# Kernel optimization log

Hardware: AMD Instinct MI355X
Metric: run time of the kernel (lower is better)

## Reference

```python
import jax, jax.numpy as jnp
import numpy as np

H = 8
DH = 64
MAX_REL = 32
SCALE = DH ** -0.5


def setup_inputs() -> dict:
    key = jax.random.key(0)
    ks = jax.random.split(key, 10)
    B, T, D = 2, 2048, 512
    s = 1.0 / np.sqrt(D)
    return {
        "hidden_states": jax.random.normal(ks[0], (B, T, D), jnp.float32),
        "Wq": jax.random.normal(ks[1], (D, H * DH), jnp.float32) * s,
        "bq": jax.random.normal(ks[2], (H * DH,), jnp.float32) * 0.02,
        "Wk": jax.random.normal(ks[3], (D, H * DH), jnp.float32) * s,
        "bk": jax.random.normal(ks[4], (H * DH,), jnp.float32) * 0.02,
        "Wv": jax.random.normal(ks[5], (D, H * DH), jnp.float32) * s,
        "bv": jax.random.normal(ks[6], (H * DH,), jnp.float32) * 0.02,
        "Wo": jax.random.normal(ks[7], (H * DH, D), jnp.float32) * s,
        "bo": jax.random.normal(ks[8], (D,), jnp.float32) * 0.02,
        "rel_bias": jax.random.normal(ks[9], (H, 2 * MAX_REL + 1), jnp.float32) * 0.02,
    }


def _rel_pos_bias(rel_bias, Tq, Tk):
    # (H, Tq, Tk) additive bias from clamped relative distances
    rel = jnp.arange(Tq)[:, None] - jnp.arange(Tk)[None, :]
    idx = jnp.clip(rel, -MAX_REL, MAX_REL) + MAX_REL
    return rel_bias[:, idx]


def reference(hidden_states, Wq, bq, Wk, bk, Wv, bv, Wo, bo, rel_bias):
    B, T, D = hidden_states.shape
    # projections (enn.Linear == dense linear map in forward math)
    Q = (hidden_states @ Wq + bq).reshape(B, T, H, DH)
    K = (hidden_states @ Wk + bk).reshape(B, T, H, DH)
    V = (hidden_states @ Wv + bv).reshape(B, T, H, DH)
    attn = jnp.einsum("bthd,bkhd->bhtk", Q, K) * SCALE
    attn = attn + _rel_pos_bias(rel_bias, T, T)[None]
    attn = jax.nn.softmax(attn, axis=-1)
    out = jnp.einsum("bhtk,bkhd->bthd", attn, V).reshape(B, T, H * DH)
    return out @ Wo + bo
```

## Files before the change

kernel.cpp:

```cpp
#include <hip/hip_runtime.h>
#include <stdint.h>
#include <math.h>

#define H 8
#define DH 64
#define T 2048
#define D 512
#define B 2
#define BH 16
#define MAXREL 32
#define NREL (2*MAXREL+1)
#define C1 0.18033688f
#define NKIT 16

typedef _Float16 half_t;
typedef half_t half8 __attribute__((ext_vector_type(8)));
typedef float f32x4 __attribute__((ext_vector_type(4)));

typedef __attribute__((address_space(3))) unsigned int lds_uint;
typedef const __attribute__((address_space(1))) unsigned int glb_uint;

__device__ __forceinline__ void gl_lds16(const void* g, void* l) {
    __builtin_amdgcn_global_load_lds((glb_uint*)g, (lds_uint*)l, 16, 0, 0);
}

__device__ __forceinline__ f32x4 zero4() { f32x4 z = {0.f, 0.f, 0.f, 0.f}; return z; }

__global__ __launch_bounds__(256) void cvt_x(const float* __restrict__ X,
                                             half_t* __restrict__ Xh) {
    const int i = (blockIdx.x * 256 + threadIdx.x) * 8;
    const float4 a = *(const float4*)(X + i);
    const float4 b = *(const float4*)(X + i + 4);
    half8 o;
    o[0]=(half_t)a.x; o[1]=(half_t)a.y; o[2]=(half_t)a.z; o[3]=(half_t)a.w;
    o[4]=(half_t)b.x; o[5]=(half_t)b.y; o[6]=(half_t)b.z; o[7]=(half_t)b.w;
    *(half8*)(Xh + i) = o;
}

__global__ __launch_bounds__(256) void trans_w(
    const float* __restrict__ Wq, const float* __restrict__ Wk,
    const float* __restrict__ Wv, const float* __restrict__ Wo,
    half_t* __restrict__ Wts) {
    const int z = blockIdx.y;
    const float* __restrict__ W = (z==0)?Wq:(z==1)?Wk:(z==2)?Wv:Wo;
    half_t* __restrict__ out = Wts + (size_t)z * (D * D);

    __shared__ half_t Ld[64 * 72];
    const int tid = threadIdx.x;
    const int k0 = (blockIdx.x >> 3) * 64;
    const int n0 = (blockIdx.x & 7) * 64;
    const int r = tid >> 2, c16 = (tid & 3) * 16;

    const float* src = W + (size_t)(k0 + r) * D + n0 + c16;
    #pragma unroll
    for (int j = 0; j < 16; ++j) Ld[r * 72 + c16 + j] = (half_t)src[j];
    __syncthreads();
    half_t tmp[16];
    #pragma unroll
    for (int j = 0; j < 16; ++j) tmp[j] = Ld[(c16 + j) * 72 + r];
    half8* dst = (half8*)(out + (size_t)(n0 + r) * D + k0 + c16);
    dst[0] = *(half8*)&tmp[0];
    dst[1] = *(half8*)&tmp[8];
}

__global__ __launch_bounds__(256) void gemm_qkv(
    const half_t* __restrict__ Xh, const half_t* __restrict__ Wts,
    const float* __restrict__ bq, const float* __restrict__ bk,
    const float* __restrict__ bv,
    half_t* __restrict__ Qh, half_t* __restrict__ Kh, half_t* __restrict__ Vh)
{
    __shared__ half_t As[64 * 32];
    __shared__ half_t Bs[128 * 32];
    const int tid = threadIdx.x, w = tid >> 6, lane = tid & 63;
    const int l15 = lane & 15, quad = lane >> 4;
    const int m0 = blockIdx.x * 64, n0 = blockIdx.y * 128, z = blockIdx.z;
    const half_t* __restrict__ Wt = Wts + (size_t)z * (D * D);
    const float* __restrict__ bias = (z==0)?bq:(z==1)?bk:bv;
    half_t* __restrict__ dst = (z==0)?Qh:(z==1)?Kh:Vh;

    f32x4 acc[4][2];
    #pragma unroll
    for (int ms = 0; ms < 4; ++ms) { acc[ms][0] = zero4(); acc[ms][1] = zero4(); }

    for (int k0 = 0; k0 < D; k0 += 32) {
        {
            const int cid = w * 64 + lane;
            gl_lds16(Xh + (size_t)(m0 + (cid >> 2)) * D + k0 + (cid & 3) * 8,
                     As + (size_t)w * 512);
            #pragma unroll
            for (int s = 0; s < 2; ++s) {
                const int cid2 = (w * 2 + s) * 64 + lane;
                gl_lds16(Wt + (size_t)(n0 + (cid2 >> 2)) * D + k0 + (cid2 & 3) * 8,
                         Bs + (size_t)(w * 2 + s) * 512);
            }
        }
        __syncthreads();
        half8 bf[2];
        #pragma unroll
        for (int nt = 0; nt < 2; ++nt)
            bf[nt] = *(const half8*)&Bs[(w * 32 + nt * 16 + l15) * 32 + quad * 8];
        #pragma unroll
        for (int ms = 0; ms < 4; ++ms) {
            const half8 af = *(const half8*)&As[(ms * 16 + l15) * 32 + quad * 8];
            acc[ms][0] = __builtin_amdgcn_mfma_f32_16x16x32_f16(af, bf[0], acc[ms][0], 0, 0, 0);
            acc[ms][1] = __builtin_amdgcn_mfma_f32_16x16x32_f16(af, bf[1], acc[ms][1], 0, 0, 0);
        }
        __syncthreads();
    }

    float bvv[2];
    #pragma unroll
    for (int nt = 0; nt < 2; ++nt) bvv[nt] = bias[n0 + w * 32 + nt * 16 + l15];
    #pragma unroll
    for (int ms = 0; ms < 4; ++ms)
        #pragma unroll
        for (int nt = 0; nt < 2; ++nt)
            #pragma unroll
            for (int r = 0; r < 4; ++r) {
                const int mrow = m0 + ms * 16 + quad * 4 + r;
                const int n = n0 + w * 32 + nt * 16 + l15;
                const int bb = mrow >> 11, t = mrow & 2047, h = n >> 6, d = n & 63;
                dst[(((size_t)bb * H + h) * T + t) * DH + d] = (half_t)(acc[ms][nt][r] + bvv[nt]);
            }
}

__global__ __launch_bounds__(256) void v_trans(const half_t* __restrict__ Vh,
                                               half_t* __restrict__ Vth) {
    __shared__ half_t Ld[64 * 72];
    const int tid = threadIdx.x;
    const int t0 = blockIdx.x * 64, bh = blockIdx.y;
    const int r = tid >> 2, c16 = (tid & 3) * 16;
    const half8* src = (const half8*)(Vh + ((size_t)bh * T + t0 + r) * DH + c16);
    *(half8*)&Ld[r * 72 + c16] = src[0];
    *(half8*)&Ld[r * 72 + c16 + 8] = src[1];
    __syncthreads();
    half_t tmp[16];
    #pragma unroll
    for (int j = 0; j < 16; ++j) tmp[j] = Ld[(c16 + j) * 72 + r];
    half8* dst = (half8*)(Vth + ((size_t)bh * DH + r) * T + t0 + c16);
    dst[0] = *(half8*)&tmp[0];
    dst[1] = *(half8*)&tmp[8];
}

__global__ __launch_bounds__(256) void attn_fwd(
    const half_t* __restrict__ Qh, const half_t* __restrict__ Kh,
    const half_t* __restrict__ Vth, const float* __restrict__ relb,
    half_t* __restrict__ Onum, half_t* __restrict__ lsum)
{
    __shared__ half_t Kt[2][4096];
    __shared__ half_t Vt[2][4096];
    __shared__ half_t Pl[4][2304];
    __shared__ float rb2[NREL];

    const int tid = threadIdx.x, w = tid >> 6, lane = tid & 63;
    const int l15 = lane & 15, quad = lane >> 4;
    const int q0 = blockIdx.x * 128;
    const int bh = blockIdx.y;
    const int split = blockIdx.z;
    const int kb0 = split * 1024;
    const int h = bh & 7;

    if (tid < NREL) rb2[tid] = relb[h * NREL + tid] * 1.44269504f;

    half8 qf[2][2];
    const half_t* Qbase = Qh + ((size_t)bh * T + q0 + w * 32) * DH;
    #pragma unroll
    for (int ms = 0; ms < 2; ++ms)
        #pragma unroll
        for (int ks = 0; ks < 2; ++ks)
            qf[ms][ks] = *(const half8*)(Qbase + (ms * 16 + l15) * DH + ks * 32 + quad * 8);

    f32x4 of[2][4];
    float lp[2][4];
    #pragma unroll
    for (int ms = 0; ms < 2; ++ms)
        #pragma unroll
        for (int nt = 0; nt < 4; ++nt) of[ms][nt] = zero4();
    #pragma unroll
    for (int ms = 0; ms < 2; ++ms)
        #pragma unroll
        for (int r = 0; r < 4; ++r) lp[ms][r] = 0.f;

    auto stage = [&](int buf, int kb) {
        #pragma unroll
        for (int s = 0; s < 2; ++s) {
            const int cid = (w * 2 + s) * 64 + lane;
            const int r = cid >> 3, cg = (cid & 7) ^ (r & 7);
            gl_lds16(Kh + ((size_t)bh * T + kb + r) * DH + cg * 8,
                     &Kt[buf][(w * 2 + s) * 512]);
            gl_lds16(Vth + ((size_t)bh * DH + r) * T + kb + cg * 8,
                     &Vt[buf][(w * 2 + s) * 512]);
        }
    };

    stage(0, kb0);
    __syncthreads();

    for (int it = 0; it < NKIT; ++it) {
        const int cur = it & 1;
        if (it + 1 < NKIT) stage(cur ^ 1, kb0 + (it + 1) * 64);
        const int kb = kb0 + it * 64;

        f32x4 sf[2][4];
        #pragma unroll
        for (int ms = 0; ms < 2; ++ms)
            #pragma unroll
            for (int nt = 0; nt < 4; ++nt) sf[ms][nt] = zero4();
        #pragma unroll
        for (int ks = 0; ks < 2; ++ks)
            #pragma unroll
            for (int nt = 0; nt < 4; ++nt) {
                const int row = nt * 16 + l15;
                const int c = ks * 4 + quad;
                const half8 kf = *(const half8*)&Kt[cur][row * 64 + ((c ^ (row & 7)) * 8)];
                sf[0][nt] = __builtin_amdgcn_mfma_f32_16x16x32_f16(qf[0][ks], kf, sf[0][nt], 0, 0, 0);
                sf[1][nt] = __builtin_amdgcn_mfma_f32_16x16x32_f16(qf[1][ks], kf, sf[1][nt], 0, 0, 0);
            }

        const bool uni_hi = (q0 - (kb + 63)) >= MAXREL;
        const bool uni_lo = ((q0 + 127) - kb) <= -MAXREL;
        if (uni_hi || uni_lo) {
            const float bu = uni_hi ? rb2[NREL - 1] : rb2[0];
            #pragma unroll
            for (int ms = 0; ms < 2; ++ms)
                #pragma unroll
                for (int nt = 0; nt < 4; ++nt)
                    #pragma unroll
                    for (int r = 0; r < 4; ++r) {
                        const float p = exp2f(fmaf(sf[ms][nt][r], C1, bu));
                        lp[ms][r] += p;
                        const int row = ms * 16 + quad * 4 + r;
                        const int col = nt * 16 + l15;
                        Pl[w][row * 72 + ((((col >> 3) ^ (row & 7)) * 8) | (col & 7))] = (half_t)p;
                    }
        } else {
            #pragma unroll
            for (int ms = 0; ms < 2; ++ms)
                #pragma unroll
                for (int nt = 0; nt < 4; ++nt)
                    #pragma unroll
                    for (int r = 0; r < 4; ++r) {
                        const int q = q0 + w * 32 + ms * 16 + quad * 4 + r;
                        const int kg = kb + nt * 16 + l15;
                        int rel = q - kg;
                        rel = rel < -MAXREL ? -MAXREL : (rel > MAXREL ? MAXREL : rel);
                        const float p = exp2f(fmaf(sf[ms][nt][r], C1, rb2[rel + MAXREL]));
                        lp[ms][r] += p;
                        const int row = ms * 16 + quad * 4 + r;
                        const int col = nt * 16 + l15;
                        Pl[w][row * 72 + ((((col >> 3) ^ (row & 7)) * 8) | (col & 7))] = (half_t)p;
                    }
        }

        #pragma unroll
        for (int ks = 0; ks < 2; ++ks) {
            half8 pf[2];
            #pragma unroll
            for (int ms = 0; ms < 2; ++ms) {
                const int row = ms * 16 + l15;
                const int c = ks * 4 + quad;
                pf[ms] = *(const half8*)&Pl[w][row * 72 + ((c ^ (row & 7)) * 8)];
            }
            #pragma unroll
            for (int nt = 0; nt < 4; ++nt) {
                const int row = nt * 16 + l15;
                const int c = ks * 4 + quad;
                const half8 vf = *(const half8*)&Vt[cur][row * 64 + ((c ^ (row & 7)) * 8)];
                of[0][nt] = __builtin_amdgcn_mfma_f32_16x16x32_f16(pf[0], vf, of[0][nt], 0, 0, 0);
                of[1][nt] = __builtin_amdgcn_mfma_f32_16x16x32_f16(pf[1], vf, of[1][nt], 0, 0, 0);
            }
        }
        __syncthreads();
    }

    const size_t obase = ((size_t)(split * BH + bh) * T + q0 + w * 32);
    #pragma unroll
    for (int ms = 0; ms < 2; ++ms)
        #pragma unroll
        for (int nt = 0; nt < 4; ++nt)
            #pragma unroll
            for (int r = 0; r < 4; ++r)
                Onum[(obase + ms * 16 + quad * 4 + r) * DH + nt * 16 + l15] =
                    (half_t)(of[ms][nt][r] * 0.015625f);

    #pragma unroll
    for (int ms = 0; ms < 2; ++ms)
        #pragma unroll
        for (int r = 0; r < 4; ++r) {
            float v = lp[ms][r];
            v += __shfl_xor(v, 1); v += __shfl_xor(v, 2);
            v += __shfl_xor(v, 4); v += __shfl_xor(v, 8);
            if (l15 == 0)
                lsum[obase + ms * 16 + quad * 4 + r] = (half_t)(v * 0.015625f);
        }
}

__global__ __launch_bounds__(256) void combine(
    const half_t* __restrict__ Onum, const half_t* __restrict__ lsum,
    half_t* __restrict__ AOh)
{
    const int i = blockIdx.x * 256 + threadIdx.x;
    const int r = i >> 6;
    const int c = (i & 63) * 8;
    const int b = r >> 11, t = r & 2047, h = c >> 6, d = c & 63;
    const int bh = b * H + h;
    const size_t o0 = ((size_t)bh * T + t) * DH + d;
    const size_t o1 = ((size_t)(BH + bh) * T + t) * DH + d;
    const half8 x0 = *(const half8*)(Onum + o0);
    const half8 x1 = *(const half8*)(Onum + o1);
    const float l = (float)lsum[(size_t)bh * T + t] + (float)lsum[(size_t)(BH + bh) * T + t];
    const float inv = 1.0f / l;
    half8 o;
    #pragma unroll
    for (int j = 0; j < 8; ++j) o[j] = (half_t)(((float)x0[j] + (float)x1[j]) * inv);
    *(half8*)(AOh + (size_t)r * D + c) = o;
}

__global__ __launch_bounds__(256) void gemm_out(
    const half_t* __restrict__ AOh, const half_t* __restrict__ Wot,
    const float* __restrict__ bo, float* __restrict__ out)
{
    __shared__ half_t As[64 * 32];
    __shared__ half_t Bs[128 * 32];
    const int tid = threadIdx.x, w = tid >> 6, lane = tid & 63;
    const int l15 = lane & 15, quad = lane >> 4;
    const int m0 = blockIdx.x * 64, n0 = blockIdx.y * 128;

    f32x4 acc[4][2];
    #pragma unroll
    for (int ms = 0; ms < 4; ++ms) { acc[ms][0] = zero4(); acc[ms][1] = zero4(); }

    for (int k0 = 0; k0 < D; k0 += 32) {
        {
            const int cid = w * 64 + lane;
            gl_lds16(AOh + (size_t)(m0 + (cid >> 2)) * D + k0 + (cid & 3) * 8,
                     As + (size_t)w * 512);
            #pragma unroll
            for (int s = 0; s < 2; ++s) {
                const int cid2 = (w * 2 + s) * 64 + lane;
                gl_lds16(Wot + (size_t)(n0 + (cid2 >> 2)) * D + k0 + (cid2 & 3) * 8,
                         Bs + (size_t)(w * 2 + s) * 512);
            }
        }
        __syncthreads();
        half8 bf[2];
        #pragma unroll
        for (int nt = 0; nt < 2; ++nt)
            bf[nt] = *(const half8*)&Bs[(w * 32 + nt * 16 + l15) * 32 + quad * 8];
        #pragma unroll
        for (int ms = 0; ms < 4; ++ms) {
            const half8 af = *(const half8*)&As[(ms * 16 + l15) * 32 + quad * 8];
            acc[ms][0] = __builtin_amdgcn_mfma_f32_16x16x32_f16(af, bf[0], acc[ms][0], 0, 0, 0);
            acc[ms][1] = __builtin_amdgcn_mfma_f32_16x16x32_f16(af, bf[1], acc[ms][1], 0, 0, 0);
        }
        __syncthreads();
    }

    float bvv[2];
    #pragma unroll
    for (int nt = 0; nt < 2; ++nt) bvv[nt] = bo[n0 + w * 32 + nt * 16 + l15];
    #pragma unroll
    for (int ms = 0; ms < 4; ++ms)
        #pragma unroll
        for (int nt = 0; nt < 2; ++nt)
            #pragma unroll
            for (int r = 0; r < 4; ++r) {
                const int mrow = m0 + ms * 16 + quad * 4 + r;
                const int n = n0 + w * 32 + nt * 16 + l15;
                out[(size_t)mrow * D + n] = acc[ms][nt][r] + bvv[nt];
            }
}

extern "C" void kernel_launch(void* const* d_in, const int* in_sizes, int n_in,
                              void* d_out, int out_size, void* d_ws, size_t ws_size,
                              hipStream_t stream)
{
    const float* hs   = (const float*)d_in[0];
    const float* Wq   = (const float*)d_in[1];
    const float* bq   = (const float*)d_in[2];
    const float* Wk   = (const float*)d_in[3];
    const float* bk   = (const float*)d_in[4];
    const float* Wv   = (const float*)d_in[5];
    const float* bv   = (const float*)d_in[6];
    const float* Wo   = (const float*)d_in[7];
    const float* bo   = (const float*)d_in[8];
    const float* relb = (const float*)d_in[9];

    const size_t NX = (size_t)B * T * D;
    const size_t NW = (size_t)D * D;
    half_t* wsh = (half_t*)d_ws;
    half_t* Xh  = wsh;
    half_t* Wts = Xh + NX;
    half_t* Wot = Wts + 3 * NW;
    half_t* Qh  = Wot + NW;
    half_t* Kh  = Qh + NX;
    half_t* Vh  = Kh + NX;
    half_t* Vth = Vh + NX;
    half_t* On  = Vth + NX;
    half_t* Ls  = On + 2 * NX;
    half_t* AOh = Vh;

    cvt_x   <<<dim3(NX / (256 * 8)), 256, 0, stream>>>(hs, Xh);
    trans_w <<<dim3(64, 4), 256, 0, stream>>>(Wq, Wk, Wv, Wo, Wts);
    gemm_qkv<<<dim3(64, 4, 3), 256, 0, stream>>>(Xh, Wts, bq, bk, bv, Qh, Kh, Vh);
    v_trans <<<dim3(32, BH), 256, 0, stream>>>(Vh, Vth);
    attn_fwd<<<dim3(16, BH, 2), 256, 0, stream>>>(Qh, Kh, Vth, relb, On, Ls);
    combine <<<dim3(1024), 256, 0, stream>>>(On, Ls, AOh);
    gemm_out<<<dim3(64, 4), 256, 0, stream>>>(AOh, Wot, bo, (float*)d_out);
}
```

Measured before the change: 152.1 us.

## Fuse prep kernels, fold V transpose into QKV GEMM, register-resident P in attention

Merges the X conversion and weight transpose into one launch and writes V directly in transposed layout from the QKV GEMM epilogue, removing the separate v_trans kernel. Both GEMMs move to double-buffered 64-wide K tiles with XOR-swizzled LDS. The output GEMM uses smaller M tiles to get more blocks. Attention computes S^T so P stays in registers and is redistributed with lane shuffles instead of a round trip through LDS, using 16 query rows per wave and twice as many blocks. The trade-offs are extra shuffle work in attention and less reuse per block in the output GEMM.

After: 147.4 us. -3.1%, faster.

```diff
diff --git a/kernel.cpp b/kernel.cpp
--- a/kernel.cpp
+++ b/kernel.cpp
@@ -11,11 +11,13 @@
 #define MAXREL 32
 #define NREL (2*MAXREL+1)
 #define C1 0.18033688f
-#define NKIT 16
+#define NW (D*D)
 
 typedef _Float16 half_t;
 typedef half_t half8 __attribute__((ext_vector_type(8)));
+typedef half_t half4 __attribute__((ext_vector_type(4)));
 typedef float f32x4 __attribute__((ext_vector_type(4)));
+typedef int int4v __attribute__((ext_vector_type(4)));
 
 typedef __attribute__((address_space(3))) unsigned int lds_uint;
 typedef const __attribute__((address_space(1))) unsigned int glb_uint;
@@ -23,123 +25,141 @@
 __device__ __forceinline__ void gl_lds16(const void* g, void* l) {
     __builtin_amdgcn_global_load_lds((glb_uint*)g, (lds_uint*)l, 16, 0, 0);
 }
-
-__device__ __forceinline__ f32x4 zero4() { f32x4 z = {0.f, 0.f, 0.f, 0.f}; return z; }
-
-__global__ __launch_bounds__(256) void cvt_x(const float* __restrict__ X,
-                                             half_t* __restrict__ Xh) {
-    const int i = (blockIdx.x * 256 + threadIdx.x) * 8;
-    const float4 a = *(const float4*)(X + i);
-    const float4 b = *(const float4*)(X + i + 4);
-    half8 o;
-    o[0]=(half_t)a.x; o[1]=(half_t)a.y; o[2]=(half_t)a.z; o[3]=(half_t)a.w;
-    o[4]=(half_t)b.x; o[5]=(half_t)b.y; o[6]=(half_t)b.z; o[7]=(half_t)b.w;
-    *(half8*)(Xh + i) = o;
-}
-
-__global__ __launch_bounds__(256) void trans_w(
+__device__ __forceinline__ f32x4 zero4() { f32x4 z = {0.f,0.f,0.f,0.f}; return z; }
+__device__ __forceinline__ int pkrtz(float a, float b) {
+    return __builtin_bit_cast(int, __builtin_amdgcn_cvt_pkrtz(a, b));
+}
+
+__global__ __launch_bounds__(256) void prep(
+    const float* __restrict__ X,
     const float* __restrict__ Wq, const float* __restrict__ Wk,
     const float* __restrict__ Wv, const float* __restrict__ Wo,
-    half_t* __restrict__ Wts) {
-    const int z = blockIdx.y;
-    const float* __restrict__ W = (z==0)?Wq:(z==1)?Wk:(z==2)?Wv:Wo;
-    half_t* __restrict__ out = Wts + (size_t)z * (D * D);
-
+    half_t* __restrict__ Xh, half_t* __restrict__ Wts)
+{
     __shared__ half_t Ld[64 * 72];
+    const int bid = blockIdx.x;
     const int tid = threadIdx.x;
-    const int k0 = (blockIdx.x >> 3) * 64;
-    const int n0 = (blockIdx.x & 7) * 64;
-    const int r = tid >> 2, c16 = (tid & 3) * 16;
-
-    const float* src = W + (size_t)(k0 + r) * D + n0 + c16;
-    #pragma unroll
-    for (int j = 0; j < 16; ++j) Ld[r * 72 + c16 + j] = (half_t)src[j];
-    __syncthreads();
-    half_t tmp[16];
-    #pragma unroll
-    for (int j = 0; j < 16; ++j) tmp[j] = Ld[(c16 + j) * 72 + r];
-    half8* dst = (half8*)(out + (size_t)(n0 + r) * D + k0 + c16);
-    dst[0] = *(half8*)&tmp[0];
-    dst[1] = *(half8*)&tmp[8];
+    if (bid < 1024) {
+        const int i = (bid * 256 + tid) * 8;
+        const float4 a = *(const float4*)(X + i);
+        const float4 b = *(const float4*)(X + i + 4);
+        half8 o;
+        o[0]=(half_t)a.x; o[1]=(half_t)a.y; o[2]=(half_t)a.z; o[3]=(half_t)a.w;
+        o[4]=(half_t)b.x; o[5]=(half_t)b.y; o[6]=(half_t)b.z; o[7]=(half_t)b.w;
+        *(half8*)(Xh + i) = o;
+    } else {
+        const int id = bid - 1024;
+        const int z = id >> 6;
+        const int tile = id & 63;
+        const float* __restrict__ W = (z==0)?Wq:(z==1)?Wk:(z==2)?Wv:Wo;
+        half_t* __restrict__ out = Wts + (size_t)z * NW;
+        const int k0 = (tile >> 3) * 64;
+        const int n0 = (tile & 7) * 64;
+        const int r = tid >> 2, c16 = (tid & 3) * 16;
+        const float* src = W + (size_t)(k0 + r) * D + n0 + c16;
+        #pragma unroll
+        for (int j = 0; j < 16; ++j) Ld[r * 72 + c16 + j] = (half_t)src[j];
+        __syncthreads();
+        half_t tmp[16];
+        #pragma unroll
+        for (int j = 0; j < 16; ++j) tmp[j] = Ld[(c16 + j) * 72 + r];
+        half8* dst = (half8*)(out + (size_t)(n0 + r) * D + k0 + c16);
+        dst[0] = *(half8*)&tmp[0];
+        dst[1] = *(half8*)&tmp[8];
+    }
 }
 
 __global__ __launch_bounds__(256) void gemm_qkv(
     const half_t* __restrict__ Xh, const half_t* __restrict__ Wts,
     const float* __restrict__ bq, const float* __restrict__ bk,
     const float* __restrict__ bv,
-    half_t* __restrict__ Qh, half_t* __restrict__ Kh, half_t* __restrict__ Vh)
-{
-    __shared__ half_t As[64 * 32];
-    __shared__ half_t Bs[128 * 32];
+    half_t* __restrict__ Qh, half_t* __restrict__ Kh, half_t* __restrict__ Vth)
+{
+    __shared__ half_t As[2][64 * 64];
+    __shared__ half_t Bs[2][128 * 64];
     const int tid = threadIdx.x, w = tid >> 6, lane = tid & 63;
     const int l15 = lane & 15, quad = lane >> 4;
     const int m0 = blockIdx.x * 64, n0 = blockIdx.y * 128, z = blockIdx.z;
-    const half_t* __restrict__ Wt = Wts + (size_t)z * (D * D);
+    const half_t* __restrict__ Wt = Wts + (size_t)z * NW;
     const float* __restrict__ bias = (z==0)?bq:(z==1)?bk:bv;
-    half_t* __restrict__ dst = (z==0)?Qh:(z==1)?Kh:Vh;
+
+    auto stage = [&](int buf, int k0) {
+        #pragma unroll
+        for (int s = 0; s < 2; ++s) {
+            const int cid = (w * 2 + s) * 64 + lane;
+            const int r = cid >> 3, c = (cid & 7) ^ (r & 7);
+            gl_lds16(Xh + (size_t)(m0 + r) * D + k0 + c * 8,
+                     &As[buf][(w * 2 + s) * 512]);
+        }
+        #pragma unroll
+        for (int s = 0; s < 4; ++s) {
+            const int cid = (w * 4 + s) * 64 + lane;
+            const int r = cid >> 3, c = (cid & 7) ^ (r & 7);
+            gl_lds16(Wt + (size_t)(n0 + r) * D + k0 + c * 8,
+                     &Bs[buf][(w * 4 + s) * 512]);
+        }
+    };
 
     f32x4 acc[4][2];
     #pragma unroll
     for (int ms = 0; ms < 4; ++ms) { acc[ms][0] = zero4(); acc[ms][1] = zero4(); }
 
-    for (int k0 = 0; k0 < D; k0 += 32) {
-        {
-            const int cid = w * 64 + lane;
-            gl_lds16(Xh + (size_t)(m0 + (cid >> 2)) * D + k0 + (cid & 3) * 8,
-                     As + (size_t)w * 512);
-            #pragma unroll
-            for (int s = 0; s < 2; ++s) {
-                const int cid2 = (w * 2 + s) * 64 + lane;
-                gl_lds16(Wt + (size_t)(n0 + (cid2 >> 2)) * D + k0 + (cid2 & 3) * 8,
-                         Bs + (size_t)(w * 2 + s) * 512);
+    stage(0, 0);
+    __syncthreads();
+    for (int it = 0; it < 8; ++it) {
+        const int cur = it & 1;
+        if (it < 7) stage(cur ^ 1, (it + 1) * 64);
+        const int swiz = l15 & 7;
+        #pragma unroll
+        for (int ks = 0; ks < 2; ++ks) {
+            const int c = (ks * 4 + quad) ^ swiz;
+            half8 bf[2];
+            #pragma unroll
+            for (int nt = 0; nt < 2; ++nt)
+                bf[nt] = *(const half8*)&Bs[cur][(w * 32 + nt * 16 + l15) * 64 + c * 8];
+            #pragma unroll
+            for (int ms = 0; ms < 4; ++ms) {
+                const half8 af = *(const half8*)&As[cur][(ms * 16 + l15) * 64 + c * 8];
+                acc[ms][0] = __builtin_amdgcn_mfma_f32_16x16x32_f16(af, bf[0], acc[ms][0], 0, 0, 0);
+                acc[ms][1] = __builtin_amdgcn_mfma_f32_16x16x32_f16(af, bf[1], acc[ms][1], 0, 0, 0);
             }
         }
         __syncthreads();
-        half8 bf[2];
-        #pragma unroll
-        for (int nt = 0; nt < 2; ++nt)
-            bf[nt] = *(const half8*)&Bs[(w * 32 + nt * 16 + l15) * 32 + quad * 8];
+    }
+
+    float bvv[2];
+    #pragma unroll
+    for (int nt = 0; nt < 2; ++nt) bvv[nt] = bias[n0 + w * 32 + nt * 16 + l15];
+
+    if (z == 2) {
         #pragma unroll
         for (int ms = 0; ms < 4; ++ms) {
-            const half8 af = *(const half8*)&As[(ms * 16 + l15) * 32 + quad * 8];
-            acc[ms][0] = __builtin_amdgcn_mfma_f32_16x16x32_f16(af, bf[0], acc[ms][0], 0, 0, 0);
-            acc[ms][1] = __builtin_amdgcn_mfma_f32_16x16x32_f16(af, bf[1], acc[ms][1], 0, 0, 0);
-        }
-        __syncthreads();
-    }
-
-    float bvv[2];
-    #pragma unroll
-    for (int nt = 0; nt < 2; ++nt) bvv[nt] = bias[n0 + w * 32 + nt * 16 + l15];
-    #pragma unroll
-    for (int ms = 0; ms < 4; ++ms)
-        #pragma unroll
-        for (int nt = 0; nt < 2; ++nt)
-            #pragma unroll
-            for (int r = 0; r < 4; ++r) {
-                const int mrow = m0 + ms * 16 + quad * 4 + r;
+            const int mbase = m0 + ms * 16 + quad * 4;
+            const int bb = mbase >> 11, t0 = mbase & 2047;
+            #pragma unroll
+            for (int nt = 0; nt < 2; ++nt) {
                 const int n = n0 + w * 32 + nt * 16 + l15;
-                const int bb = mrow >> 11, t = mrow & 2047, h = n >> 6, d = n & 63;
-                dst[(((size_t)bb * H + h) * T + t) * DH + d] = (half_t)(acc[ms][nt][r] + bvv[nt]);
-            }
-}
-
-__global__ __launch_bounds__(256) void v_trans(const half_t* __restrict__ Vh,
-                                               half_t* __restrict__ Vth) {
-    __shared__ half_t Ld[64 * 72];
-    const int tid = threadIdx.x;
-    const int t0 = blockIdx.x * 64, bh = blockIdx.y;
-    const int r = tid >> 2, c16 = (tid & 3) * 16;
-    const half8* src = (const half8*)(Vh + ((size_t)bh * T + t0 + r) * DH + c16);
-    *(half8*)&Ld[r * 72 + c16] = src[0];
-    *(half8*)&Ld[r * 72 + c16 + 8] = src[1];
-    __syncthreads();
-    half_t tmp[16];
-    #pragma unroll
-    for (int j = 0; j < 16; ++j) tmp[j] = Ld[(c16 + j) * 72 + r];
-    half8* dst = (half8*)(Vth + ((size_t)bh * DH + r) * T + t0 + c16);
-    dst[0] = *(half8*)&tmp[0];
-    dst[1] = *(half8*)&tmp[8];
+                const int hh = n >> 6, d = n & 63;
+                half4 pk;
+                #pragma unroll
+                for (int r = 0; r < 4; ++r) pk[r] = (half_t)(acc[ms][nt][r] + bvv[nt]);
+                *(half4*)(Vth + (((size_t)bb * H + hh) * DH + d) * T + t0) = pk;
+            }
+        }
+    } else {
+        half_t* __restrict__ dst = (z == 0) ? Qh : Kh;
+        #pragma unroll
+        for (int ms = 0; ms < 4; ++ms)
+            #pragma unroll
+            for (int nt = 0; nt < 2; ++nt)
+                #pragma unroll
+                for (int r = 0; r < 4; ++r) {
+                    const int mrow = m0 + ms * 16 + quad * 4 + r;
+                    const int n = n0 + w * 32 + nt * 16 + l15;
+                    const int bb = mrow >> 11, t = mrow & 2047, hh = n >> 6, d = n & 63;
+                    dst[(((size_t)bb * H + hh) * T + t) * DH + d] = (half_t)(acc[ms][nt][r] + bvv[nt]);
+                }
+    }
 }
 
 __global__ __launch_bounds__(256) void attn_fwd(
@@ -149,12 +169,12 @@
 {
     __shared__ half_t Kt[2][4096];
     __shared__ half_t Vt[2][4096];
-    __shared__ half_t Pl[4][2304];
     __shared__ float rb2[NREL];
 
     const int tid = threadIdx.x, w = tid >> 6, lane = tid & 63;
     const int l15 = lane & 15, quad = lane >> 4;
-    const int q0 = blockIdx.x * 128;
+    const int q0 = blockIdx.x * 64;
+    const int qw = q0 + w * 16;
     const int bh = blockIdx.y;
     const int split = blockIdx.z;
     const int kb0 = split * 1024;
@@ -162,24 +182,16 @@
 
     if (tid < NREL) rb2[tid] = relb[h * NREL + tid] * 1.44269504f;
 
-    half8 qf[2][2];
-    const half_t* Qbase = Qh + ((size_t)bh * T + q0 + w * 32) * DH;
-    #pragma unroll
-    for (int ms = 0; ms < 2; ++ms)
-        #pragma unroll
-        for (int ks = 0; ks < 2; ++ks)
-            qf[ms][ks] = *(const half8*)(Qbase + (ms * 16 + l15) * DH + ks * 32 + quad * 8);
-
-    f32x4 of[2][4];
-    float lp[2][4];
-    #pragma unroll
-    for (int ms = 0; ms < 2; ++ms)
-        #pragma unroll
-        for (int nt = 0; nt < 4; ++nt) of[ms][nt] = zero4();
-    #pragma unroll
-    for (int ms = 0; ms < 2; ++ms)
-        #pragma unroll
-        for (int r = 0; r < 4; ++r) lp[ms][r] = 0.f;
+    half8 qf[2];
+    const half_t* Qbase = Qh + ((size_t)bh * T + qw) * DH;
+    #pragma unroll
+    for (int ks = 0; ks < 2; ++ks)
+        qf[ks] = *(const half8*)(Qbase + l15 * DH + ks * 32 + quad * 8);
+
+    f32x4 of[4];
+    #pragma unroll
+    for (int nt = 0; nt < 4; ++nt) of[nt] = zero4();
+    float lp = 0.f;
 
     auto stage = [&](int buf, int kb) {
         #pragma unroll
@@ -196,103 +208,91 @@
     stage(0, kb0);
     __syncthreads();
 
-    for (int it = 0; it < NKIT; ++it) {
+    const int qg = qw + l15;
+    const int swiz = l15 & 7;
+
+    for (int it = 0; it < 16; ++it) {
         const int cur = it & 1;
-        if (it + 1 < NKIT) stage(cur ^ 1, kb0 + (it + 1) * 64);
+        if (it + 1 < 16) stage(cur ^ 1, kb0 + (it + 1) * 64);
         const int kb = kb0 + it * 64;
 
-        f32x4 sf[2][4];
-        #pragma unroll
-        for (int ms = 0; ms < 2; ++ms)
-            #pragma unroll
-            for (int nt = 0; nt < 4; ++nt) sf[ms][nt] = zero4();
-        #pragma unroll
-        for (int ks = 0; ks < 2; ++ks)
+        f32x4 st[4];
+        #pragma unroll
+        for (int nt = 0; nt < 4; ++nt) st[nt] = zero4();
+        #pragma unroll
+        for (int ks = 0; ks < 2; ++ks) {
+            const int c = (ks * 4 + quad) ^ swiz;
             #pragma unroll
             for (int nt = 0; nt < 4; ++nt) {
-                const int row = nt * 16 + l15;
-                const int c = ks * 4 + quad;
-                const half8 kf = *(const half8*)&Kt[cur][row * 64 + ((c ^ (row & 7)) * 8)];
-                sf[0][nt] = __builtin_amdgcn_mfma_f32_16x16x32_f16(qf[0][ks], kf, sf[0][nt], 0, 0, 0);
-                sf[1][nt] = __builtin_amdgcn_mfma_f32_16x16x32_f16(qf[1][ks], kf, sf[1][nt], 0, 0, 0);
-            }
-
-        const bool uni_hi = (q0 - (kb + 63)) >= MAXREL;
-        const bool uni_lo = ((q0 + 127) - kb) <= -MAXREL;
+                const half8 kf = *(const half8*)&Kt[cur][(nt * 16 + l15) * 64 + c * 8];
+                st[nt] = __builtin_amdgcn_mfma_f32_16x16x32_f16(kf, qf[ks], st[nt], 0, 0, 0);
+            }
+        }
+
+        int pd[4][2];
+        const bool uni_hi = (qw - (kb + 63)) >= MAXREL;
+        const bool uni_lo = ((qw + 15) - kb) <= -MAXREL;
         if (uni_hi || uni_lo) {
             const float bu = uni_hi ? rb2[NREL - 1] : rb2[0];
             #pragma unroll
-            for (int ms = 0; ms < 2; ++ms)
+            for (int nt = 0; nt < 4; ++nt) {
+                float p[4];
                 #pragma unroll
-                for (int nt = 0; nt < 4; ++nt)
-                    #pragma unroll
-                    for (int r = 0; r < 4; ++r) {
-                        const float p = exp2f(fmaf(sf[ms][nt][r], C1, bu));
-                        lp[ms][r] += p;
-                        const int row = ms * 16 + quad * 4 + r;
-                        const int col = nt * 16 + l15;
-                        Pl[w][row * 72 + ((((col >> 3) ^ (row & 7)) * 8) | (col & 7))] = (half_t)p;
-                    }
+                for (int r = 0; r < 4; ++r) p[r] = exp2f(fmaf(st[nt][r], C1, bu));
+                lp += (p[0] + p[1]) + (p[2] + p[3]);
+                pd[nt][0] = pkrtz(p[0], p[1]);
+                pd[nt][1] = pkrtz(p[2], p[3]);
+            }
         } else {
             #pragma unroll
-            for (int ms = 0; ms < 2; ++ms)
+            for (int nt = 0; nt < 4; ++nt) {
+                float p[4];
                 #pragma unroll
-                for (int nt = 0; nt < 4; ++nt)
-                    #pragma unroll
-                    for (int r = 0; r < 4; ++r) {
-                        const int q = q0 + w * 32 + ms * 16 + quad * 4 + r;
-                        const int kg = kb + nt * 16 + l15;
-                        int rel = q - kg;
-                        rel = rel < -MAXREL ? -MAXREL : (rel > MAXREL ? MAXREL : rel);
-                        const float p = exp2f(fmaf(sf[ms][nt][r], C1, rb2[rel + MAXREL]));
-                        lp[ms][r] += p;
-                        const int row = ms * 16 + quad * 4 + r;
-                        const int col = nt * 16 + l15;
-                        Pl[w][row * 72 + ((((col >> 3) ^ (row & 7)) * 8) | (col & 7))] = (half_t)p;
-                    }
+                for (int r = 0; r < 4; ++r) {
+                    const int key = kb + nt * 16 + quad * 4 + r;
+                    int rel = qg - key;
+                    rel = rel < -MAXREL ? -MAXREL : (rel > MAXREL ? MAXREL : rel);
+                    p[r] = exp2f(fmaf(st[nt][r], C1, rb2[rel + MAXREL]));
+                }
+                lp += (p[0] + p[1]) + (p[2] + p[3]);
+                pd[nt][0] = pkrtz(p[0], p[1]);
+                pd[nt][1] = pkrtz(p[2], p[3]);
+            }
         }
 
         #pragma unroll
         for (int ks = 0; ks < 2; ++ks) {
-            half8 pf[2];
-            #pragma unroll
-            for (int ms = 0; ms < 2; ++ms) {
-                const int row = ms * 16 + l15;
-                const int c = ks * 4 + quad;
-                pf[ms] = *(const half8*)&Pl[w][row * 72 + ((c ^ (row & 7)) * 8)];
-            }
+            int4v bd;
+            #pragma unroll
+            for (int d = 0; d < 4; ++d) {
+                const int src = ((quad & 1) * 2 + (d >> 1)) * 16 + l15;
+                const int va = __shfl(pd[2 * ks][d & 1], src);
+                const int vb = __shfl(pd[2 * ks + 1][d & 1], src);
+                bd[d] = (quad >> 1) ? vb : va;
+            }
+            const half8 pf = __builtin_bit_cast(half8, bd);
+            const int c = (ks * 4 + quad) ^ swiz;
             #pragma unroll
             for (int nt = 0; nt < 4; ++nt) {
-                const int row = nt * 16 + l15;
-                const int c = ks * 4 + quad;
-                const half8 vf = *(const half8*)&Vt[cur][row * 64 + ((c ^ (row & 7)) * 8)];
-                of[0][nt] = __builtin_amdgcn_mfma_f32_16x16x32_f16(pf[0], vf, of[0][nt], 0, 0, 0);
-                of[1][nt] = __builtin_amdgcn_mfma_f32_16x16x32_f16(pf[1], vf, of[1][nt], 0, 0, 0);
+                const half8 vf = *(const half8*)&Vt[cur][(nt * 16 + l15) * 64 + c * 8];
+                of[nt] = __builtin_amdgcn_mfma_f32_16x16x32_f16(vf, pf, of[nt], 0, 0, 0);
             }
         }
         __syncthreads();
     }
 
-    const size_t obase = ((size_t)(split * BH + bh) * T + q0 + w * 32);
-    #pragma unroll
-    for (int ms = 0; ms < 2; ++ms)
-        #pragma unroll
-        for (int nt = 0; nt < 4; ++nt)
-            #pragma unroll
-            for (int r = 0; r < 4; ++r)
-                Onum[(obase + ms * 16 + quad * 4 + r) * DH + nt * 16 + l15] =
-                    (half_t)(of[ms][nt][r] * 0.015625f);
-
-    #pragma unroll
-    for (int ms = 0; ms < 2; ++ms)
-        #pragma unroll
-        for (int r = 0; r < 4; ++r) {
-            float v = lp[ms][r];
-            v += __shfl_xor(v, 1); v += __shfl_xor(v, 2);
-            v += __shfl_xor(v, 4); v += __shfl_xor(v, 8);
-            if (l15 == 0)
-                lsum[obase + ms * 16 + quad * 4 + r] = (half_t)(v * 0.015625f);
-        }
+    const size_t qrow = (size_t)(split * BH + bh) * T + qw + l15;
+    half_t* obase = Onum + qrow * DH;
+    #pragma unroll
+    for (int nt = 0; nt < 4; ++nt) {
+        half4 pk;
+        #pragma unroll
+        for (int r = 0; r < 4; ++r) pk[r] = (half_t)(of[nt][r] * 0.015625f);
+        *(half4*)(obase + nt * 16 + quad * 4) = pk;
+    }
+    lp += __shfl_xor(lp, 16);
+    lp += __shfl_xor(lp, 32);
+    if (quad == 0) lsum[qrow] = (half_t)(lp * 0.015625f);
 }
 
 __global__ __launch_bounds__(256) void combine(
@@ -302,8 +302,8 @@
     const int i = blockIdx.x * 256 + threadIdx.x;
     const int r = i >> 6;
     const int c = (i & 63) * 8;
-    const int b = r >> 11, t = r & 2047, h = c >> 6, d = c & 63;
-    const int bh = b * H + h;
+    const int b = r >> 11, t = r & 2047, hh = c >> 6, d = c & 63;
+    const int bh = b * H + hh;
     const size_t o0 = ((size_t)bh * T + t) * DH + d;
     const size_t o1 = ((size_t)(BH + bh) * T + t) * DH + d;
     const half8 x0 = *(const half8*)(Onum + o0);
@@ -320,47 +320,60 @@
     const half_t* __restrict__ AOh, const half_t* __restrict__ Wot,
     const float* __restrict__ bo, float* __restrict__ out)
 {
-    __shared__ half_t As[64 * 32];
-    __shared__ half_t Bs[128 * 32];
+    __shared__ half_t As[2][32 * 64];
+    __shared__ half_t Bs[2][128 * 64];
     const int tid = threadIdx.x, w = tid >> 6, lane = tid & 63;
     const int l15 = lane & 15, quad = lane >> 4;
-    const int m0 = blockIdx.x * 64, n0 = blockIdx.y * 128;
-
-    f32x4 acc[4][2];
-    #pragma unroll
-    for (int ms = 0; ms < 4; ++ms) { acc[ms][0] = zero4(); acc[ms][1] = zero4(); }
-
-    for (int k0 = 0; k0 < D; k0 += 32) {
+    const int m0 = blockIdx.x * 32, n0 = blockIdx.y * 128;
+
+    auto stage = [&](int buf, int k0) {
         {
             const int cid = w * 64 + lane;
-            gl_lds16(AOh + (size_t)(m0 + (cid >> 2)) * D + k0 + (cid & 3) * 8,
-                     As + (size_t)w * 512);
-            #pragma unroll
-            for (int s = 0; s < 2; ++s) {
-                const int cid2 = (w * 2 + s) * 64 + lane;
-                gl_lds16(Wot + (size_t)(n0 + (cid2 >> 2)) * D + k0 + (cid2 & 3) * 8,
-                         Bs + (size_t)(w * 2 + s) * 512);
+            const int r = cid >> 3, c = (cid & 7) ^ (r & 7);
+            gl_lds16(AOh + (size_t)(m0 + r) * D + k0 + c * 8,
+                     &As[buf][w * 512]);
+        }
+        #pragma unroll
+        for (int s = 0; s < 4; ++s) {
+            const int cid = (w * 4 + s) * 64 + lane;
+            const int r = cid >> 3, c = (cid & 7) ^ (r & 7);
+            gl_lds16(Wot + (size_t)(n0 + r) * D + k0 + c * 8,
+                     &Bs[buf][(w * 4 + s) * 512]);
+        }
+    };
+
+    f32x4 acc[2][2];
+    #pragma unroll
+    for (int ms = 0; ms < 2; ++ms) { acc[ms][0] = zero4(); acc[ms][1] = zero4(); }
+
+    stage(0, 0);
+    __syncthreads();
+    for (int it = 0; it < 8; ++it) {
+        const int cur = it & 1;
+        if (it < 7) stage(cur ^ 1, (it + 1) * 64);
+        const int swiz = l15 & 7;
+        #pragma unroll
+        for (int ks = 0; ks < 2; ++ks) {
+            const int c = (ks * 4 + quad) ^ swiz;
+            half8 bf[2];
+            #pragma unroll
+            for (int nt = 0; nt < 2; ++nt)
+                bf[nt] = *(const half8*)&Bs[cur][(w * 32 + nt * 16 + l15) * 64 + c * 8];
+            #pragma unroll
+            for (int ms = 0; ms < 2; ++ms) {
+                const half8 af = *(const half8*)&As[cur][(ms * 16 + l15) * 64 + c * 8];
+                acc[ms][0] = __builtin_amdgcn_mfma_f32_16x16x32_f16(af, bf[0], acc[ms][0], 0, 0, 0);
+                acc[ms][1] = __builtin_amdgcn_mfma_f32_16x16x32_f16(af, bf[1], acc[ms][1], 0, 0, 0);
             }
         }
         __syncthreads();
-        half8 bf[2];
-        #pragma unroll
-        for (int nt = 0; nt < 2; ++nt)
-            bf[nt] = *(const half8*)&Bs[(w * 32 + nt * 16 + l15) * 32 + quad * 8];
-        #pragma unroll
-        for (int ms = 0; ms < 4; ++ms) {
-            const half8 af = *(const half8*)&As[(ms * 16 + l15) * 32 + quad * 8];
-            acc[ms][0] = __builtin_amdgcn_mfma_f32_16x16x32_f16(af, bf[0], acc[ms][0], 0, 0, 0);
-            acc[ms][1] = __builtin_amdgcn_mfma_f32_16x16x32_f16(af, bf[1], acc[ms][1], 0, 0, 0);
-        }
-        __syncthreads();
     }
 
     float bvv[2];
     #pragma unroll
     for (int nt = 0; nt < 2; ++nt) bvv[nt] = bo[n0 + w * 32 + nt * 16 + l15];
     #pragma unroll
-    for (int ms = 0; ms < 4; ++ms)
+    for (int ms = 0; ms < 2; ++ms)
         #pragma unroll
         for (int nt = 0; nt < 2; ++nt)
             #pragma unroll
@@ -387,24 +400,19 @@
     const float* relb = (const float*)d_in[9];
 
     const size_t NX = (size_t)B * T * D;
-    const size_t NW = (size_t)D * D;
     half_t* wsh = (half_t*)d_ws;
     half_t* Xh  = wsh;
     half_t* Wts = Xh + NX;
-    half_t* Wot = Wts + 3 * NW;
-    half_t* Qh  = Wot + NW;
+    half_t* Qh  = Wts + 4 * (size_t)NW;
     half_t* Kh  = Qh + NX;
-    half_t* Vh  = Kh + NX;
-    half_t* Vth = Vh + NX;
+    half_t* Vth = Kh + NX;
     half_t* On  = Vth + NX;
     half_t* Ls  = On + 2 * NX;
-    half_t* AOh = Vh;
-
-    cvt_x   <<<dim3(NX / (256 * 8)), 256, 0, stream>>>(hs, Xh);
-    trans_w <<<dim3(64, 4), 256, 0, stream>>>(Wq, Wk, Wv, Wo, Wts);
-    gemm_qkv<<<dim3(64, 4, 3), 256, 0, stream>>>(Xh, Wts, bq, bk, bv, Qh, Kh, Vh);
-    v_trans <<<dim3(32, BH), 256, 0, stream>>>(Vh, Vth);
-    attn_fwd<<<dim3(16, BH, 2), 256, 0, stream>>>(Qh, Kh, Vth, relb, On, Ls);
+    half_t* AOh = Ls + 2 * BH * T;
+
+    prep    <<<dim3(1280), 256, 0, stream>>>(hs, Wq, Wk, Wv, Wo, Xh, Wts);
+    gemm_qkv<<<dim3(64, 4, 3), 256, 0, stream>>>(Xh, Wts, bq, bk, bv, Qh, Kh, Vth);
+    attn_fwd<<<dim3(32, BH, 2), 256, 0, stream>>>(Qh, Kh, Vth, relb, On, Ls);
     combine <<<dim3(1024), 256, 0, stream>>>(On, Ls, AOh);
-    gemm_out<<<dim3(64, 4), 256, 0, stream>>>(AOh, Wot, bo, (float*)d_out);
-}
+    gemm_out<<<dim3(128, 4), 256, 0, stream>>>(AOh, Wts + 3 * (size_t)NW, bo, (float*)d_out);
+}
```
